# Optimization experiments

Measured on AMD Instinct MI355X. Metric: run time of the kernel, lower is better.

Reference implementation:

```python
import jax, jax.numpy as jnp
import numpy as np

N, E, C, D, A, F_, H, RNF = 20000, 200000, 14, 3, 16, 128, 128, 128
CONSTANT = 1.0
LN_EPS = 1e-5


def _pool_matrix(n_channel, dtype):
    ones = np.ones((n_channel, n_channel))
    mats = []
    for i in range(n_channel):
        ws = n_channel - i
        mats.append((np.triu(ones) - np.triu(ones, k=ws)) / ws)
    return jnp.asarray(np.stack(mats), dtype)  # [C, C, C]


def _scatter_mean(src, idx, n):
    s = jax.ops.segment_sum(src, idx, num_segments=n)
    cnt = jax.ops.segment_sum(jnp.ones((src.shape[0],), src.dtype), idx, num_segments=n)
    return s / jnp.maximum(cnt, 1.0).reshape((n,) + (1,) * (src.ndim - 1))


def setup_inputs() -> dict:
    key = jax.random.key(0)
    ks = jax.random.split(key, 24)
    h = jax.random.normal(ks[0], (N, F_), jnp.float32)
    x = jax.random.normal(ks[1], (N, C, D), jnp.float32)
    channel_attr = jax.random.normal(ks[2], (N, C, A), jnp.float32)
    cw = jax.random.uniform(ks[3], (N, C), jnp.float32)
    cw = cw * (jax.random.uniform(ks[4], (N, C)) > 0.3)  # some padded channels
    cw = cw.at[:, 0].set(jax.random.uniform(ks[5], (N,)) + 0.1)  # >=1 valid channel
    row = jax.random.randint(ks[6], (E,), 0, N, dtype=jnp.int32)
    col = jax.random.randint(ks[7], (E,), 0, N, dtype=jnp.int32)

    def lin(k, din, dout):
        return 0.02 * jax.random.normal(k, (din, dout), jnp.float32), jnp.zeros((dout,), jnp.float32)

    rad_w, rad_b = lin(ks[8], A * A, RNF)
    e_w1, e_b1 = lin(ks[9], 2 * F_ + RNF, H)
    e_w2, e_b2 = lin(ks[10], H, H)
    att_w, att_b = lin(ks[11], H, 1)
    c_w1, c_b1 = lin(ks[12], H, H)
    c_w2, c_b2 = lin(ks[13], H, C)
    n_w1, n_b1 = lin(ks[14], F_ + H, H)
    n_w2, n_b2 = lin(ks[15], H, F_)
    ln_g = jnp.ones((F_,), jnp.float32)
    ln_b = jnp.zeros((F_,), jnp.float32)
    return dict(h=h, x=x, channel_attr=channel_attr, channel_weights=cw, row=row, col=col,
                rad_w=rad_w, rad_b=rad_b, e_w1=e_w1, e_b1=e_b1, e_w2=e_w2, e_b2=e_b2,
                att_w=att_w, att_b=att_b, c_w1=c_w1, c_b1=c_b1, c_w2=c_w2, c_b2=c_b2,
                n_w1=n_w1, n_b1=n_b1, n_w2=n_w2, n_b2=n_b2, ln_g=ln_g, ln_b=ln_b)


def reference(h, x, channel_attr, channel_weights, row, col,
              rad_w, rad_b, e_w1, e_b1, e_w2, e_b2, att_w, att_b,
              c_w1, c_b1, c_w2, c_b2, n_w1, n_b1, n_w2, n_b2, ln_g, ln_b):
    silu = jax.nn.silu
    n_nodes = h.shape[0]

    # ---- coord2radial (NUM_SEG = 1) ----
    # pairwise channel distances per edge: [E, C, C]
    coord_msg = jnp.linalg.norm(x[row][:, :, None, :] - x[col][:, None, :, :], axis=-1)
    coord_msg = coord_msg * (channel_weights[row][:, :, None] * channel_weights[col][:, None, :])
    # attr^T @ msg @ attr -> [E, A, A] -> [E, A*A]
    radial = jnp.einsum('eca,ecd,edb->eab', channel_attr[row], coord_msg, channel_attr[col])
    radial = radial.reshape(radial.shape[0], -1)
    radial_norm = jnp.linalg.norm(radial, axis=-1, keepdims=True) + CONSTANT
    radial = (radial @ rad_w + rad_b) / radial_norm

    channel_mask = (channel_weights != 0).astype(x.dtype)  # [N, C]
    channel_sum = jnp.sum(channel_weights != 0, axis=-1).astype(jnp.int32)  # [N]
    pooled_col = (x[col] * channel_mask[col][:, :, None]).sum(1) / channel_sum[col].astype(x.dtype)[:, None]
    coord_diff = x[row] - pooled_col[:, None, :]  # [E, C, 3]

    # ---- edge MLP + attention gate ----
    ef = silu(jnp.concatenate([h[row], h[col], radial], axis=-1) @ e_w1 + e_b1)
    ef = silu(ef @ e_w2 + e_b2)
    ef = ef * jax.nn.sigmoid(ef @ att_w + att_b)  # att_mlp active (hidden_nf == input_nf)

    # ---- RollerPooling on coord_mlp output ----
    cm = silu(ef @ c_w1 + c_b1) @ c_w2 + c_b2  # [E, C]
    pool_mat = _pool_matrix(C, ef.dtype)[channel_sum[row] - 1]  # [E, C, C]
    pooled = jnp.einsum('eij,ej->ei', pool_mat, cm)  # [E, C]
    trans = coord_diff * pooled[:, :, None]  # [E, C, 3]

    x_new = x + _scatter_mean(trans, row, n_nodes)
    agg = _scatter_mean(ef, col, n_nodes)

    nh = silu(jnp.concatenate([h, agg], axis=-1) @ n_w1 + n_b1) @ n_w2 + n_b2
    hr = h + nh
    mu = hr.mean(-1, keepdims=True)
    var = ((hr - mu) ** 2).mean(-1, keepdims=True)
    h_new = (hr - mu) * jax.lax.rsqrt(var + LN_EPS) * ln_g + ln_b
    return h_new, x_new
```

## Files before the change

kernel.cpp:

```cpp
#include <hip/hip_runtime.h>
#include <hip/hip_bf16.h>


#define TM 64
#define TN 16
#define PAD 36

typedef __attribute__((ext_vector_type(8))) short bf16x8;
typedef __attribute__((ext_vector_type(4))) short bf16x4;
typedef __attribute__((ext_vector_type(4))) float f32x4;

__device__ __forceinline__ float siluf(float v) { return v / (1.f + __expf(-v)); }
__device__ __forceinline__ float sigmf(float v) { return 1.f / (1.f + __expf(-v)); }
__device__ __forceinline__ short f2bs(float f) {
  union { __hip_bfloat16 b; short s; } u;
  u.b = __float2bfloat16(f);
  return u.s;
}
__device__ __forceinline__ __hip_bfloat162 mk_bf162(float v0, float v1) {
  __hip_bfloat162 r;
  r.x = __float2bfloat16(v0);
  r.y = __float2bfloat16(v1);
  return r;
}

__global__ __launch_bounds__(256) void k_pack(
    const float* __restrict__ h, const float* __restrict__ x,
    const float* __restrict__ attr, const float* __restrict__ cw,
    const float* __restrict__ rad_w, const float* __restrict__ e_w1,
    const float* __restrict__ e_w2, const float* __restrict__ c_w1,
    const float* __restrict__ n_w1, const float* __restrict__ n_w2,
    const float* __restrict__ c_w2,
    __hip_bfloat16* __restrict__ wz_rad, __hip_bfloat16* __restrict__ wz_e1,
    __hip_bfloat16* __restrict__ wz_e2, __hip_bfloat16* __restrict__ wz_c1,
    __hip_bfloat16* __restrict__ wz_n1, __hip_bfloat16* __restrict__ wz_n2,
    __hip_bfloat16* __restrict__ wz_c2,
    __hip_bfloat16* __restrict__ attrS, __hip_bfloat16* __restrict__ hb,
    float* __restrict__ pooled_x, int* __restrict__ chsum, int Nn) {
  int idx = blockIdx.x * 256 + threadIdx.x;
  if (idx < 165888) {
    int i = idx;
    if (i >= 163840) {
      int base = i - 163840;
      int k = base >> 4, n = base & 15;
      wz_c2[(size_t)(k >> 5) * 512 + n * 32 + (k & 31)] =
          (n < 14) ? __float2bfloat16(c_w2[k * 14 + n]) : __float2bfloat16(0.f);
      return;
    }
    const float* W;
    __hip_bfloat16* O;
    int base;
    if (i < 32768) { W = rad_w; O = wz_rad; base = i; }
    else if (i < 81920) { W = e_w1; O = wz_e1; base = i - 32768; }
    else if (i < 98304) { W = e_w2; O = wz_e2; base = i - 81920; }
    else if (i < 114688) { W = c_w1; O = wz_c1; base = i - 98304; }
    else if (i < 147456) { W = n_w1; O = wz_n1; base = i - 114688; }
    else { W = n_w2; O = wz_n2; base = i - 147456; }
    int k = base >> 7, n = base & 127;
    int nr_ = ((n >> 5) << 5) | ((n & 1) << 4) | ((n & 31) >> 1);
    O[(size_t)((k >> 5) * 128 + nr_) * 32 + (k & 31)] = __float2bfloat16(W[base]);
    return;
  }
  idx -= 165888;
  int na = Nn * 256, nh = Nn * 128;
  if (idx < na) {
    int n = idx >> 8, r = idx & 255, i2 = r >> 4, a = r & 15;
    float v = 0.f;
    if (i2 < 14) v = attr[(size_t)n * 224 + i2 * 16 + a] * cw[(size_t)n * 14 + i2];
    attrS[(size_t)n * 256 + a * 16 + i2] = __float2bfloat16(v);
    return;
  }
  idx -= na;
  if (idx < nh) {
    hb[idx] = __float2bfloat16(h[idx]);
    return;
  }
  idx -= nh;
  if (idx >= Nn) return;
  int n = idx;
  int cnt = 0;
  float sx = 0.f, sy = 0.f, sz = 0.f;
#pragma unroll
  for (int c = 0; c < 14; c++) {
    float w = cw[n * 14 + c];
    if (w != 0.f) {
      cnt++;
      sx += x[n * 42 + c * 3 + 0];
      sy += x[n * 42 + c * 3 + 1];
      sz += x[n * 42 + c * 3 + 2];
    }
  }
  chsum[n] = cnt;
  float inv = 1.f / (float)(cnt > 0 ? cnt : 1);
  pooled_x[n * 3 + 0] = sx * inv;
  pooled_x[n * 3 + 1] = sy * inv;
  pooled_x[n * 3 + 2] = sz * inv;
}

__global__ __launch_bounds__(256, 3) void k_mega(
    const __hip_bfloat16* __restrict__ hb, const float* __restrict__ x,
    const __hip_bfloat16* __restrict__ attrS,
    const int* __restrict__ row, const int* __restrict__ col,
    const float* __restrict__ pooled_x, const int* __restrict__ chsum,
    const __hip_bfloat16* __restrict__ wz_rad, const float* __restrict__ rad_b,
    const __hip_bfloat16* __restrict__ wz_e1, const float* __restrict__ e_b1,
    const __hip_bfloat16* __restrict__ wz_e2, const float* __restrict__ e_b2,
    const float* __restrict__ att_w, const float* __restrict__ att_b,
    const __hip_bfloat16* __restrict__ wz_c1, const float* __restrict__ c_b1,
    const __hip_bfloat16* __restrict__ wz_c2, const float* __restrict__ c_b2,
    unsigned* __restrict__ cnt_row, unsigned* __restrict__ cnt_col,
    __hip_bfloat162* __restrict__ x_acc, __hip_bfloat162* __restrict__ agg,
    int Ee) {
  __shared__ __hip_bfloat16 S[12][TM][32];
  __shared__ float s_att[TM];
  __shared__ float s_red[4][TM];
  __shared__ float s_rn[TM];
  __shared__ int s_row[TM], s_col[TM], s_cs[TM];
  float* s_cm   = (float*)&S[0][0][0];
  float* s_pool = (float*)&S[1][0][0];

  const int t = threadIdx.x;
  const int e0 = blockIdx.x * TM;
  const int ne = min(TM, Ee - e0);
  const int lane = t & 63, wave = t >> 6, quad = lane >> 4, mr = lane & 15;
  const int n0 = wave * 32;
  const f32x4 zacc = {0.f, 0.f, 0.f, 0.f};
  const bf16x4 zero4 = {0, 0, 0, 0};

  if (t < TM) {
    int ge = e0 + min(t, ne - 1);
    int r = row[ge], c = col[ge];
    s_row[t] = r;
    s_col[t] = c;
    s_cs[t] = chsum[r];
    if (t < ne) {
      atomicAdd(&cnt_row[r], 1u);
      atomicAdd(&cnt_col[c], 1u);
    }
  }

#pragma unroll 1
  for (int b = 0; b < 4; b++) {
    float xr0v[4], xr1v[4], xr2v[4], xc0v[4], xc1v[4], xc2v[4];
    bf16x4 bCv[4], aRv[4];
#pragma unroll
    for (int p = 0; p < 4; p++) {
      const int e = wave * 16 + b * 4 + p;
      const int ge = e0 + min(e, ne - 1);
      const int re = row[ge], ce = col[ge];
      const int mrc = min(mr, 13);
      const float* xp = x + (size_t)re * 42 + mrc * 3;
      xr0v[p] = xp[0]; xr1v[p] = xp[1]; xr2v[p] = xp[2];
      const float* xq = x + (size_t)ce * 42 + mrc * 3;
      xc0v[p] = xq[0]; xc1v[p] = xq[1]; xc2v[p] = xq[2];
      bCv[p] = *(const bf16x4*)&attrS[(size_t)ce * 256 + mr * 16 + quad * 4];
      aRv[p] = *(const bf16x4*)&attrS[(size_t)re * 256 + mr * 16 + quad * 4];
    }
#pragma unroll
    for (int p = 0; p < 4; p++) {
      const int e = wave * 16 + b * 4 + p;
      const float xr0 = xr0v[p], xr1 = xr1v[p], xr2 = xr2v[p];
      const float xc0 = xc0v[p], xc1 = xc1v[p], xc2 = xc2v[p];
      const float nr = xr0 * xr0 + xr1 * xr1 + xr2 * xr2;
      const float nc = xc0 * xc0 + xc1 * xc1 + xc2 * xc2;
      bf16x4 aX = zero4, bX = zero4;
      if (quad == 0) {
        aX[0] = f2bs(xc0); aX[1] = f2bs(xc1); aX[2] = f2bs(xc2);
        bX[0] = f2bs(xr0); bX[1] = f2bs(xr1); bX[2] = f2bs(xr2);
      }
      f32x4 G = __builtin_amdgcn_mfma_f32_16x16x16bf16_1k(aX, bX, zacc, 0, 0, 0);
      bf16x4 aM;
#pragma unroll
      for (int r = 0; r < 4; r++) {
        float ncj = __shfl(nc, quad * 4 + r);
        aM[r] = f2bs(sqrtf(fmaxf(ncj + nr - 2.f * G[r], 0.f)));
      }
      f32x4 m1 = __builtin_amdgcn_mfma_f32_16x16x16bf16_1k(aM, bCv[p], zacc, 0, 0, 0);
      bf16x4 bM;
#pragma unroll
      for (int r = 0; r < 4; r++) bM[r] = f2bs(m1[r]);
      f32x4 rd = __builtin_amdgcn_mfma_f32_16x16x16bf16_1k(aRv[p], bM, zacc, 0, 0, 0);
      float ss = rd[0] * rd[0] + rd[1] * rd[1] + rd[2] * rd[2] + rd[3] * rd[3];
      ss += __shfl_xor(ss, 32); ss += __shfl_xor(ss, 16); ss += __shfl_xor(ss, 8);
      ss += __shfl_xor(ss, 4);  ss += __shfl_xor(ss, 2);  ss += __shfl_xor(ss, 1);
      if (lane == 0) s_rn[e] = sqrtf(ss) + 1.0f;
#pragma unroll
      for (int r = 0; r < 4; r++) {
        const int aa = quad * 4 + r;
        const int c = ((aa & 1) << 4) | mr;
        const int pcol = (((c >> 3) ^ ((e >> 1) & 3)) << 3) | (c & 7);
        S[aa >> 1][e][pcol] = __float2bfloat16(rd[r]);
      }
    }
  }
  __syncthreads();

  const int acol = ((quad ^ ((mr >> 1) & 3)) << 3);
  const int m2 = 2 * mr;

  {
    f32x4 a0[4], a1[4];
#pragma unroll
    for (int mf = 0; mf < 4; mf++) { a0[mf] = zacc; a1[mf] = zacc; }
#pragma unroll
    for (int kb = 0; kb < 8; kb++) {
      const __hip_bfloat16* wp = wz_rad + ((size_t)(kb * 128 + n0 + mr) * 32 + quad * 8);
      bf16x8 b0 = *(const bf16x8*)wp;
      bf16x8 b1 = *(const bf16x8*)(wp + 16 * 32);
#pragma unroll
      for (int mf = 0; mf < 4; mf++) {
        bf16x8 a = *(const bf16x8*)&S[kb][mf * 16 + mr][acol];
        a0[mf] = __builtin_amdgcn_mfma_f32_16x16x32_bf16(a, b0, a0[mf], 0, 0, 0);
        a1[mf] = __builtin_amdgcn_mfma_f32_16x16x32_bf16(a, b1, a1[mf], 0, 0, 0);
      }
    }
    const float2 rbp = *(const float2*)&rad_b[n0 + m2];
#pragma unroll
    for (int mf = 0; mf < 4; mf++)
#pragma unroll
      for (int r = 0; r < 4; r++) {
        int e = mf * 16 + quad * 4 + r;
        int pc2 = ((((m2) >> 3) ^ ((e >> 1) & 3)) << 3) | (m2 & 7);
        float inv = 1.f / s_rn[e];
        *(__hip_bfloat162*)&S[8 + wave][e][pc2] =
            mk_bf162((a0[mf][r] + rbp.x) * inv, (a1[mf][r] + rbp.y) * inv);
      }
  }
  __syncthreads();

  {
    const int m = t >> 2, part = t & 3;
    const int pc = ((part ^ ((m >> 1) & 3)) << 3);
    const __hip_bfloat16* hr = hb + (size_t)s_row[m] * 128 + part * 8;
    const __hip_bfloat16* hc = hb + (size_t)s_col[m] * 128 + part * 8;
#pragma unroll
    for (int kb = 0; kb < 4; kb++) {
      *(int4*)&S[kb][m][pc]     = *(const int4*)&hr[kb * 32];
      *(int4*)&S[4 + kb][m][pc] = *(const int4*)&hc[kb * 32];
    }
  }
  __syncthreads();

  f32x4 s1a0[4], s1a1[4];
#pragma unroll
  for (int mf = 0; mf < 4; mf++) { s1a0[mf] = zacc; s1a1[mf] = zacc; }
#pragma unroll
  for (int kb = 0; kb < 12; kb++) {
    const __hip_bfloat16* wp = wz_e1 + ((size_t)(kb * 128 + n0 + mr) * 32 + quad * 8);
    bf16x8 b0 = *(const bf16x8*)wp;
    bf16x8 b1 = *(const bf16x8*)(wp + 16 * 32);
#pragma unroll
    for (int mf = 0; mf < 4; mf++) {
      bf16x8 a = *(const bf16x8*)&S[kb][mf * 16 + mr][acol];
      s1a0[mf] = __builtin_amdgcn_mfma_f32_16x16x32_bf16(a, b0, s1a0[mf], 0, 0, 0);
      s1a1[mf] = __builtin_amdgcn_mfma_f32_16x16x32_bf16(a, b1, s1a1[mf], 0, 0, 0);
    }
  }
  __syncthreads();
  {
    const float2 b1p = *(const float2*)&e_b1[n0 + m2];
#pragma unroll
    for (int mf = 0; mf < 4; mf++)
#pragma unroll
      for (int r = 0; r < 4; r++) {
        int e = mf * 16 + quad * 4 + r;
        int pc2 = (((m2 >> 3) ^ ((e >> 1) & 3)) << 3) | (m2 & 7);
        *(__hip_bfloat162*)&S[wave][e][pc2] =
            mk_bf162(siluf(s1a0[mf][r] + b1p.x), siluf(s1a1[mf][r] + b1p.y));
      }
  }
  __syncthreads();

  const float2 awp = *(const float2*)&att_w[n0 + m2];
  {
    f32x4 a0[4], a1[4];
#pragma unroll
    for (int mf = 0; mf < 4; mf++) { a0[mf] = zacc; a1[mf] = zacc; }
#pragma unroll
    for (int kb = 0; kb < 4; kb++) {
      const __hip_bfloat16* wp = wz_e2 + ((size_t)(kb * 128 + n0 + mr) * 32 + quad * 8);
      bf16x8 b0 = *(const bf16x8*)wp;
      bf16x8 b1 = *(const bf16x8*)(wp + 16 * 32);
#pragma unroll
      for (int mf = 0; mf < 4; mf++) {
        bf16x8 a = *(const bf16x8*)&S[kb][mf * 16 + mr][acol];
        a0[mf] = __builtin_amdgcn_mfma_f32_16x16x32_bf16(a, b0, a0[mf], 0, 0, 0);
        a1[mf] = __builtin_amdgcn_mfma_f32_16x16x32_bf16(a, b1, a1[mf], 0, 0, 0);
      }
    }
    const float2 b2p = *(const float2*)&e_b2[n0 + m2];
    float part[4][4];
#pragma unroll
    for (int mf = 0; mf < 4; mf++)
#pragma unroll
      for (int r = 0; r < 4; r++) {
        int e = mf * 16 + quad * 4 + r;
        int pc2 = (((m2 >> 3) ^ ((e >> 1) & 3)) << 3) | (m2 & 7);
        float v0 = siluf(a0[mf][r] + b2p.x);
        float v1 = siluf(a1[mf][r] + b2p.y);
        *(__hip_bfloat162*)&S[4 + wave][e][pc2] = mk_bf162(v0, v1);
        part[mf][r] = v0 * awp.x + v1 * awp.y;
      }
#pragma unroll
    for (int msk = 1; msk < 16; msk <<= 1)
#pragma unroll
      for (int mf = 0; mf < 4; mf++)
#pragma unroll
        for (int r = 0; r < 4; r++) part[mf][r] += __shfl_xor(part[mf][r], msk);
    if (mr == 0) {
#pragma unroll
      for (int mf = 0; mf < 4; mf++)
#pragma unroll
        for (int r = 0; r < 4; r++)
          s_red[wave][mf * 16 + quad * 4 + r] = part[mf][r];
    }
  }
  __syncthreads();
  if (t < TM) {
    float s = s_red[0][t] + s_red[1][t] + s_red[2][t] + s_red[3][t];
    s_att[t] = sigmf(s + att_b[0]);
  }
  __syncthreads();

  {
    f32x4 a0[4], a1[4];
#pragma unroll
    for (int mf = 0; mf < 4; mf++) { a0[mf] = zacc; a1[mf] = zacc; }
#pragma unroll
    for (int kb = 0; kb < 4; kb++) {
      const __hip_bfloat16* wp = wz_c1 + ((size_t)(kb * 128 + n0 + mr) * 32 + quad * 8);
      bf16x8 b0 = *(const bf16x8*)wp;
      bf16x8 b1 = *(const bf16x8*)(wp + 16 * 32);
#pragma unroll
      for (int mf = 0; mf < 4; mf++) {
        bf16x8 a = *(const bf16x8*)&S[4 + kb][mf * 16 + mr][acol];
        a0[mf] = __builtin_amdgcn_mfma_f32_16x16x32_bf16(a, b0, a0[mf], 0, 0, 0);
        a1[mf] = __builtin_amdgcn_mfma_f32_16x16x32_bf16(a, b1, a1[mf], 0, 0, 0);
      }
    }
    const float2 cbp = *(const float2*)&c_b1[n0 + m2];
#pragma unroll
    for (int mf = 0; mf < 4; mf++)
#pragma unroll
      for (int r = 0; r < 4; r++) {
        int e = mf * 16 + quad * 4 + r;
        int pc2 = (((m2 >> 3) ^ ((e >> 1) & 3)) << 3) | (m2 & 7);
        float av = s_att[e];
        *(__hip_bfloat162*)&S[8 + wave][e][pc2] =
            mk_bf162(siluf(av * a0[mf][r] + cbp.x), siluf(av * a1[mf][r] + cbp.y));
      }
  }
  __syncthreads();

  {
    f32x4 acc = zacc;
#pragma unroll
    for (int kb = 0; kb < 4; kb++) {
      bf16x8 a = *(const bf16x8*)&S[8 + kb][wave * 16 + mr][acol];
      bf16x8 b = *(const bf16x8*)(wz_c2 + ((size_t)(kb * 16 + mr) * 32 + quad * 8));
      acc = __builtin_amdgcn_mfma_f32_16x16x32_bf16(a, b, acc, 0, 0, 0);
    }
    if (mr < 14) {
      float bias = c_b2[mr];
#pragma unroll
      for (int r = 0; r < 4; r++)
        s_cm[(wave * 16 + quad * 4 + r) * 14 + mr] = acc[r] + bias;
    }
  }
  __syncthreads();

  for (int i = t; i < TM * 14; i += 256) {
    int e = i / 14, c = i % 14;
    int wsz = 15 - s_cs[e];
    int hi = min(c + wsz, 14);
    float s = 0.f;
    for (int j = c; j < hi; j++) s += s_cm[e * 14 + j];
    s_pool[e * 14 + c] = s / (float)wsz;
  }
  __syncthreads();

  for (int i = t; i < TM * 21; i += 256) {
    int e = i / 21, pr = i % 21;
    if (e < ne) {
      int r0 = pr * 2, r1 = r0 + 1;
      const float* xp = x + (size_t)s_row[e] * 42;
      const float* pc = pooled_x + (size_t)s_col[e] * 3;
      float v0 = (xp[r0] - pc[r0 % 3]) * s_pool[e * 14 + r0 / 3];
      float v1 = (xp[r1] - pc[r1 % 3]) * s_pool[e * 14 + r1 / 3];
      unsafeAtomicAdd(&x_acc[(size_t)s_row[e] * 21 + pr], mk_bf162(v0, v1));
    }
  }
  for (int i = t; i < TM * 64; i += 256) {
    int e = i >> 6, o2 = i & 63;
    if (e < ne) {
      float av = s_att[e];
      int c = (o2 & 15) * 2;
      int pc = (((c >> 3) ^ ((e >> 1) & 3)) << 3) | (c & 7);
      const __hip_bfloat16* wp2 = &S[4 + (o2 >> 4)][e][pc];
      float v0 = __bfloat162float(wp2[0]) * av;
      float v1 = __bfloat162float(wp2[1]) * av;
      unsafeAtomicAdd(&agg[(size_t)s_col[e] * 64 + o2], mk_bf162(v0, v1));
    }
  }
}

__global__ __launch_bounds__(256) void k_node(
    const float* __restrict__ h, const __hip_bfloat162* __restrict__ agg,
    const unsigned* __restrict__ cnt_col,
    const __hip_bfloat16* __restrict__ wz_n1, const float* __restrict__ n_b1,
    const __hip_bfloat16* __restrict__ wz_n2, const float* __restrict__ n_b2,
    const float* __restrict__ ln_g, const float* __restrict__ ln_b,
    const float* __restrict__ x, const __hip_bfloat162* __restrict__ x_acc,
    const unsigned* __restrict__ cnt_row,
    float* __restrict__ out_h, float* __restrict__ out_x, int Nn) {
  __shared__ __hip_bfloat16 sA[8][16][PAD];
  __shared__ __hip_bfloat16 sT[4][16][PAD];
  __shared__ float s_h[TN][128];
  __shared__ float s_o[TN][132];
  const int t = threadIdx.x;
  const int nb0 = blockIdx.x * TN;
  const int nn = min(TN, Nn - nb0);

  for (int i = t; i < TN * 21; i += 256) {
    int n = i / 21, pr = i % 21;
    if (n < nn) {
      int gn = nb0 + n;
      unsigned c = cnt_row[gn];
      float inv = 1.f / (float)(c > 0 ? c : 1);
      float2 xa = __bfloat1622float2(x_acc[(size_t)gn * 21 + pr]);
      size_t gi = (size_t)gn * 42 + pr * 2;
      out_x[gi]     = x[gi] + xa.x * inv;
      out_x[gi + 1] = x[gi + 1] + xa.y * inv;
    }
  }

  for (int i = t; i < TN * 64; i += 256) {
    int m = i >> 6, kp = (i & 63) << 1;
    int kb = kp >> 5, kk = kp & 31;
    int gn = nb0 + min(m, nn - 1);
    const float2 hv = *(const float2*)&h[(size_t)gn * 128 + kp];
    sA[kb][m][kk]     = __float2bfloat16(hv.x);
    sA[kb][m][kk + 1] = __float2bfloat16(hv.y);
    s_h[m][kp]     = hv.x;
    s_h[m][kp + 1] = hv.y;
    unsigned c = cnt_col[gn];
    float inv = 1.f / (float)(c > 0 ? c : 1);
    float2 gv = __bfloat1622float2(agg[(size_t)gn * 64 + (kp >> 1)]);
    sA[4 + kb][m][kk]     = __float2bfloat16(gv.x * inv);
    sA[4 + kb][m][kk + 1] = __float2bfloat16(gv.y * inv);
  }
  __syncthreads();
  const int lane = t & 63, wave = t >> 6, quad = lane >> 4, mr = lane & 15;
  const int n0 = wave * 32;
  const int m2 = 2 * mr;
  f32x4 zacc = {0.f, 0.f, 0.f, 0.f};
  {
    f32x4 acc0 = zacc, acc1 = zacc;
#pragma unroll
    for (int kb = 0; kb < 8; kb++) {
      bf16x8 a = *(const bf16x8*)&sA[kb][mr][quad * 8];
      const __hip_bfloat16* wp = wz_n1 + ((size_t)(kb * 128 + n0 + mr) * 32 + quad * 8);
      bf16x8 b0 = *(const bf16x8*)wp;
      bf16x8 b1 = *(const bf16x8*)(wp + 16 * 32);
      acc0 = __builtin_amdgcn_mfma_f32_16x16x32_bf16(a, b0, acc0, 0, 0, 0);
      acc1 = __builtin_amdgcn_mfma_f32_16x16x32_bf16(a, b1, acc1, 0, 0, 0);
    }
    const float2 b1p = *(const float2*)&n_b1[n0 + m2];
#pragma unroll
    for (int r = 0; r < 4; r++) {
      int m = quad * 4 + r;
      *(__hip_bfloat162*)&sT[wave][m][m2] =
          mk_bf162(siluf(acc0[r] + b1p.x), siluf(acc1[r] + b1p.y));
    }
  }
  __syncthreads();
  {
    f32x4 acc0 = zacc, acc1 = zacc;
#pragma unroll
    for (int kb = 0; kb < 4; kb++) {
      bf16x8 a = *(const bf16x8*)&sT[kb][mr][quad * 8];
      const __hip_bfloat16* wp = wz_n2 + ((size_t)(kb * 128 + n0 + mr) * 32 + quad * 8);
      bf16x8 b0 = *(const bf16x8*)wp;
      bf16x8 b1 = *(const bf16x8*)(wp + 16 * 32);
      acc0 = __builtin_amdgcn_mfma_f32_16x16x32_bf16(a, b0, acc0, 0, 0, 0);
      acc1 = __builtin_amdgcn_mfma_f32_16x16x32_bf16(a, b1, acc1, 0, 0, 0);
    }
    const float2 b2p = *(const float2*)&n_b2[n0 + m2];
#pragma unroll
    for (int r = 0; r < 4; r++) {
      int m = quad * 4 + r;
      s_o[m][n0 + m2]     = s_h[m][n0 + m2] + acc0[r] + b2p.x;
      s_o[m][n0 + m2 + 1] = s_h[m][n0 + m2 + 1] + acc1[r] + b2p.y;
    }
  }
  __syncthreads();
  {
    int n = t >> 4, p = t & 15;
    float v[8];
    float s = 0.f;
#pragma unroll
    for (int j = 0; j < 8; j++) {
      v[j] = s_o[n][p * 8 + j];
      s += v[j];
    }
    s += __shfl_xor(s, 1); s += __shfl_xor(s, 2);
    s += __shfl_xor(s, 4); s += __shfl_xor(s, 8);
    float mu = s * (1.f / 128.f);
    float var = 0.f;
#pragma unroll
    for (int j = 0; j < 8; j++) {
      float d = v[j] - mu;
      var += d * d;
    }
    var += __shfl_xor(var, 1); var += __shfl_xor(var, 2);
    var += __shfl_xor(var, 4); var += __shfl_xor(var, 8);
    float rs = rsqrtf(var * (1.f / 128.f) + 1e-5f);
    if (n < nn) {
      size_t base = (size_t)(nb0 + n) * 128 + p * 8;
#pragma unroll
      for (int j = 0; j < 8; j++)
        out_h[base + j] = (v[j] - mu) * rs * ln_g[p * 8 + j] + ln_b[p * 8 + j];
    }
  }
}

extern "C" void kernel_launch(void* const* d_in, const int* in_sizes, int n_in,
                              void* d_out, int out_size, void* d_ws, size_t ws_size,
                              hipStream_t stream) {
  const float* h     = (const float*)d_in[0];
  const float* x     = (const float*)d_in[1];
  const float* attr  = (const float*)d_in[2];
  const float* cw    = (const float*)d_in[3];
  const int*   row   = (const int*)d_in[4];
  const int*   col   = (const int*)d_in[5];
  const float* rad_w = (const float*)d_in[6];
  const float* rad_b = (const float*)d_in[7];
  const float* e_w1  = (const float*)d_in[8];
  const float* e_b1  = (const float*)d_in[9];
  const float* e_w2  = (const float*)d_in[10];
  const float* e_b2  = (const float*)d_in[11];
  const float* att_w = (const float*)d_in[12];
  const float* att_b = (const float*)d_in[13];
  const float* c_w1  = (const float*)d_in[14];
  const float* c_b1  = (const float*)d_in[15];
  const float* c_w2  = (const float*)d_in[16];
  const float* c_b2  = (const float*)d_in[17];
  const float* n_w1  = (const float*)d_in[18];
  const float* n_b1  = (const float*)d_in[19];
  const float* n_w2  = (const float*)d_in[20];
  const float* n_b2  = (const float*)d_in[21];
  const float* ln_g  = (const float*)d_in[22];
  const float* ln_b  = (const float*)d_in[23];

  const int N = in_sizes[0] / 128;
  const int E = in_sizes[4];

  char* ws = (char*)d_ws;
  size_t off = 0;
  auto alloc = [&](size_t bytes) {
    size_t o = off;
    off += (bytes + 255) & ~(size_t)255;
    return o;
  };
  size_t off_wzr  = alloc(32768 * sizeof(__hip_bfloat16));
  size_t off_wz1  = alloc(49152 * sizeof(__hip_bfloat16));
  size_t off_wz2  = alloc(16384 * sizeof(__hip_bfloat16));
  size_t off_wzc  = alloc(16384 * sizeof(__hip_bfloat16));
  size_t off_wzn1 = alloc(32768 * sizeof(__hip_bfloat16));
  size_t off_wzn2 = alloc(16384 * sizeof(__hip_bfloat16));
  size_t off_wzc2 = alloc(2048 * sizeof(__hip_bfloat16));
  size_t off_atS  = alloc((size_t)N * 256 * sizeof(__hip_bfloat16));
  size_t off_hb   = alloc((size_t)N * 128 * sizeof(__hip_bfloat16));
  size_t off_px   = alloc((size_t)N * 3 * sizeof(float));
  size_t off_cs   = alloc((size_t)N * sizeof(int));
  size_t off_cntr = alloc((size_t)N * sizeof(unsigned));
  size_t off_cntc = alloc((size_t)N * sizeof(unsigned));
  size_t off_xacc = alloc((size_t)N * 21 * sizeof(__hip_bfloat162));
  size_t off_agg  = alloc((size_t)N * 64 * sizeof(__hip_bfloat162));

  __hip_bfloat16* wz_rad = (__hip_bfloat16*)(ws + off_wzr);
  __hip_bfloat16* wz_e1  = (__hip_bfloat16*)(ws + off_wz1);
  __hip_bfloat16* wz_e2  = (__hip_bfloat16*)(ws + off_wz2);
  __hip_bfloat16* wz_c1  = (__hip_bfloat16*)(ws + off_wzc);
  __hip_bfloat16* wz_n1  = (__hip_bfloat16*)(ws + off_wzn1);
  __hip_bfloat16* wz_n2  = (__hip_bfloat16*)(ws + off_wzn2);
  __hip_bfloat16* wz_c2  = (__hip_bfloat16*)(ws + off_wzc2);
  __hip_bfloat16* attrS  = (__hip_bfloat16*)(ws + off_atS);
  __hip_bfloat16* hb     = (__hip_bfloat16*)(ws + off_hb);
  float* pooled_x   = (float*)(ws + off_px);
  int* chsum        = (int*)(ws + off_cs);
  unsigned* cnt_row = (unsigned*)(ws + off_cntr);
  unsigned* cnt_col = (unsigned*)(ws + off_cntc);
  __hip_bfloat162* x_acc = (__hip_bfloat162*)(ws + off_xacc);
  __hip_bfloat162* agg   = (__hip_bfloat162*)(ws + off_agg);

  (void)hipMemsetAsync(ws + off_cntr, 0, off - off_cntr, stream);

  const int pack_items = 165888 + N * 256 + N * 128 + N;
  k_pack<<<dim3((pack_items + 255) / 256), dim3(256), 0, stream>>>(
      h, x, attr, cw, rad_w, e_w1, e_w2, c_w1, n_w1, n_w2, c_w2,
      wz_rad, wz_e1, wz_e2, wz_c1, wz_n1, wz_n2, wz_c2,
      attrS, hb, pooled_x, chsum, N);
  k_mega<<<dim3((E + TM - 1) / TM), dim3(256), 0, stream>>>(
      hb, x, attrS, row, col, pooled_x, chsum,
      wz_rad, rad_b, wz_e1, e_b1, wz_e2, e_b2, att_w, att_b,
      wz_c1, c_b1, wz_c2, c_b2, cnt_row, cnt_col, x_acc, agg, E);
  k_node<<<dim3((N + TN - 1) / TN), dim3(256), 0, stream>>>(
      h, agg, cnt_col, wz_n1, n_b1, wz_n2, n_b2, ln_g, ln_b,
      x, x_acc, cnt_row, (float*)d_out, (float*)d_out + (size_t)N * 128, N);
}
```

Baseline: 349.9 us.

## Enlarge node-kernel tile to 64 rows with swizzled LDS and vectorize pack

The node kernel now processes 64 nodes per block instead of 16, so each loaded weight fragment feeds four MFMA row tiles. It reads prepacked bf16 h from the workspace, uses one XOR-swizzled shared buffer that is reused for the fp32 output, and re-reads h from global memory for the residual add. The pack kernel's attribute and h conversions now write 8 bf16 per thread with 128-bit stores. This aims to cut weight traffic, LDS footprint and thread count in the small kernels, at the cost of more registers per thread and fewer node blocks.

```diff
diff --git a/kernel.cpp b/kernel.cpp
--- a/kernel.cpp
+++ b/kernel.cpp
@@ -3,8 +3,7 @@
 
 
 #define TM 64
-#define TN 16
-#define PAD 36
+#define TN 64
 
 typedef __attribute__((ext_vector_type(8))) short bf16x8;
 typedef __attribute__((ext_vector_type(4))) short bf16x4;
@@ -62,17 +61,31 @@
     return;
   }
   idx -= 165888;
-  int na = Nn * 256, nh = Nn * 128;
+  int na = Nn * 32, nh = Nn * 16;
   if (idx < na) {
-    int n = idx >> 8, r = idx & 255, i2 = r >> 4, a = r & 15;
-    float v = 0.f;
-    if (i2 < 14) v = attr[(size_t)n * 224 + i2 * 16 + a] * cw[(size_t)n * 14 + i2];
-    attrS[(size_t)n * 256 + a * 16 + i2] = __float2bfloat16(v);
+    int n = idx >> 5, r = idx & 31, a = r >> 1, h8 = r & 1;
+    __hip_bfloat16 outv[8];
+#pragma unroll
+    for (int j = 0; j < 8; j++) {
+      int i2 = h8 * 8 + j;
+      float v = 0.f;
+      if (i2 < 14) v = attr[(size_t)n * 224 + i2 * 16 + a] * cw[(size_t)n * 14 + i2];
+      outv[j] = __float2bfloat16(v);
+    }
+    *(int4*)&attrS[(size_t)n * 256 + a * 16 + h8 * 8] = *(int4*)outv;
     return;
   }
   idx -= na;
   if (idx < nh) {
-    hb[idx] = __float2bfloat16(h[idx]);
+    int n = idx >> 4, q = idx & 15;
+    const float4 f0 = *(const float4*)&h[(size_t)n * 128 + q * 8];
+    const float4 f1 = *(const float4*)&h[(size_t)n * 128 + q * 8 + 4];
+    __hip_bfloat16 outv[8];
+    outv[0] = __float2bfloat16(f0.x); outv[1] = __float2bfloat16(f0.y);
+    outv[2] = __float2bfloat16(f0.z); outv[3] = __float2bfloat16(f0.w);
+    outv[4] = __float2bfloat16(f1.x); outv[5] = __float2bfloat16(f1.y);
+    outv[6] = __float2bfloat16(f1.z); outv[7] = __float2bfloat16(f1.w);
+    *(int4*)&hb[(size_t)n * 128 + q * 8] = *(int4*)outv;
     return;
   }
   idx -= nh;
@@ -404,8 +417,9 @@
   }
 }
 
-__global__ __launch_bounds__(256) void k_node(
-    const float* __restrict__ h, const __hip_bfloat162* __restrict__ agg,
+__global__ __launch_bounds__(256, 3) void k_node(
+    const float* __restrict__ h, const __hip_bfloat16* __restrict__ hb,
+    const __hip_bfloat162* __restrict__ agg,
     const unsigned* __restrict__ cnt_col,
     const __hip_bfloat16* __restrict__ wz_n1, const float* __restrict__ n_b1,
     const __hip_bfloat16* __restrict__ wz_n2, const float* __restrict__ n_b2,
@@ -413,13 +427,16 @@
     const float* __restrict__ x, const __hip_bfloat162* __restrict__ x_acc,
     const unsigned* __restrict__ cnt_row,
     float* __restrict__ out_h, float* __restrict__ out_x, int Nn) {
-  __shared__ __hip_bfloat16 sA[8][16][PAD];
-  __shared__ __hip_bfloat16 sT[4][16][PAD];
-  __shared__ float s_h[TN][128];
-  __shared__ float s_o[TN][132];
+  __shared__ __hip_bfloat16 S[12][TN][32];
+  float* s_o = (float*)&S[0][0][0];
+
   const int t = threadIdx.x;
   const int nb0 = blockIdx.x * TN;
   const int nn = min(TN, Nn - nb0);
+  const int lane = t & 63, wave = t >> 6, quad = lane >> 4, mr = lane & 15;
+  const int n0 = wave * 32;
+  const int m2 = 2 * mr;
+  const f32x4 zacc = {0.f, 0.f, 0.f, 0.f};
 
   for (int i = t; i < TN * 21; i += 256) {
     int n = i / 21, pr = i % 21;
@@ -434,73 +451,104 @@
     }
   }
 
-  for (int i = t; i < TN * 64; i += 256) {
-    int m = i >> 6, kp = (i & 63) << 1;
-    int kb = kp >> 5, kk = kp & 31;
-    int gn = nb0 + min(m, nn - 1);
-    const float2 hv = *(const float2*)&h[(size_t)gn * 128 + kp];
-    sA[kb][m][kk]     = __float2bfloat16(hv.x);
-    sA[kb][m][kk + 1] = __float2bfloat16(hv.y);
-    s_h[m][kp]     = hv.x;
-    s_h[m][kp + 1] = hv.y;
+  {
+    const int m = t >> 2, part = t & 3;
+    const int gn = nb0 + min(m, nn - 1);
+    const int pc = ((part ^ ((m >> 1) & 3)) << 3);
+    const __hip_bfloat16* hr = hb + (size_t)gn * 128 + part * 8;
     unsigned c = cnt_col[gn];
     float inv = 1.f / (float)(c > 0 ? c : 1);
-    float2 gv = __bfloat1622float2(agg[(size_t)gn * 64 + (kp >> 1)]);
-    sA[4 + kb][m][kk]     = __float2bfloat16(gv.x * inv);
-    sA[4 + kb][m][kk + 1] = __float2bfloat16(gv.y * inv);
-  }
-  __syncthreads();
-  const int lane = t & 63, wave = t >> 6, quad = lane >> 4, mr = lane & 15;
-  const int n0 = wave * 32;
-  const int m2 = 2 * mr;
-  f32x4 zacc = {0.f, 0.f, 0.f, 0.f};
-  {
-    f32x4 acc0 = zacc, acc1 = zacc;
+    const __hip_bfloat162* ag = agg + (size_t)gn * 64 + part * 4;
+#pragma unroll
+    for (int kb = 0; kb < 4; kb++) {
+      *(int4*)&S[kb][m][pc] = *(const int4*)&hr[kb * 32];
+      float2 f0 = __bfloat1622float2(ag[kb * 16 + 0]);
+      float2 f1 = __bfloat1622float2(ag[kb * 16 + 1]);
+      float2 f2 = __bfloat1622float2(ag[kb * 16 + 2]);
+      float2 f3 = __bfloat1622float2(ag[kb * 16 + 3]);
+      __hip_bfloat162 pk[4];
+      pk[0] = mk_bf162(f0.x * inv, f0.y * inv);
+      pk[1] = mk_bf162(f1.x * inv, f1.y * inv);
+      pk[2] = mk_bf162(f2.x * inv, f2.y * inv);
+      pk[3] = mk_bf162(f3.x * inv, f3.y * inv);
+      *(int4*)&S[4 + kb][m][pc] = *(int4*)pk;
+    }
+  }
+  __syncthreads();
+
+  const int acol = ((quad ^ ((mr >> 1) & 3)) << 3);
+
+  {
+    f32x4 a0[4], a1[4];
+#pragma unroll
+    for (int mf = 0; mf < 4; mf++) { a0[mf] = zacc; a1[mf] = zacc; }
 #pragma unroll
     for (int kb = 0; kb < 8; kb++) {
-      bf16x8 a = *(const bf16x8*)&sA[kb][mr][quad * 8];
       const __hip_bfloat16* wp = wz_n1 + ((size_t)(kb * 128 + n0 + mr) * 32 + quad * 8);
       bf16x8 b0 = *(const bf16x8*)wp;
       bf16x8 b1 = *(const bf16x8*)(wp + 16 * 32);
-      acc0 = __builtin_amdgcn_mfma_f32_16x16x32_bf16(a, b0, acc0, 0, 0, 0);
-      acc1 = __builtin_amdgcn_mfma_f32_16x16x32_bf16(a, b1, acc1, 0, 0, 0);
+#pragma unroll
+      for (int mf = 0; mf < 4; mf++) {
+        bf16x8 a = *(const bf16x8*)&S[kb][mf * 16 + mr][acol];
+        a0[mf] = __builtin_amdgcn_mfma_f32_16x16x32_bf16(a, b0, a0[mf], 0, 0, 0);
+        a1[mf] = __builtin_amdgcn_mfma_f32_16x16x32_bf16(a, b1, a1[mf], 0, 0, 0);
+      }
     }
     const float2 b1p = *(const float2*)&n_b1[n0 + m2];
 #pragma unroll
-    for (int r = 0; r < 4; r++) {
-      int m = quad * 4 + r;
-      *(__hip_bfloat162*)&sT[wave][m][m2] =
-          mk_bf162(siluf(acc0[r] + b1p.x), siluf(acc1[r] + b1p.y));
-    }
-  }
-  __syncthreads();
-  {
-    f32x4 acc0 = zacc, acc1 = zacc;
+    for (int mf = 0; mf < 4; mf++)
+#pragma unroll
+      for (int r = 0; r < 4; r++) {
+        int e = mf * 16 + quad * 4 + r;
+        int pc2 = (((m2 >> 3) ^ ((e >> 1) & 3)) << 3) | (m2 & 7);
+        *(__hip_bfloat162*)&S[8 + wave][e][pc2] =
+            mk_bf162(siluf(a0[mf][r] + b1p.x), siluf(a1[mf][r] + b1p.y));
+      }
+  }
+  __syncthreads();
+
+  {
+    f32x4 a0[4], a1[4];
+#pragma unroll
+    for (int mf = 0; mf < 4; mf++) { a0[mf] = zacc; a1[mf] = zacc; }
 #pragma unroll
     for (int kb = 0; kb < 4; kb++) {
-      bf16x8 a = *(const bf16x8*)&sT[kb][mr][quad * 8];
       const __hip_bfloat16* wp = wz_n2 + ((size_t)(kb * 128 + n0 + mr) * 32 + quad * 8);
       bf16x8 b0 = *(const bf16x8*)wp;
       bf16x8 b1 = *(const bf16x8*)(wp + 16 * 32);
-      acc0 = __builtin_amdgcn_mfma_f32_16x16x32_bf16(a, b0, acc0, 0, 0, 0);
-      acc1 = __builtin_amdgcn_mfma_f32_16x16x32_bf16(a, b1, acc1, 0, 0, 0);
+#pragma unroll
+      for (int mf = 0; mf < 4; mf++) {
+        bf16x8 a = *(const bf16x8*)&S[8 + kb][mf * 16 + mr][acol];
+        a0[mf] = __builtin_amdgcn_mfma_f32_16x16x32_bf16(a, b0, a0[mf], 0, 0, 0);
+        a1[mf] = __builtin_amdgcn_mfma_f32_16x16x32_bf16(a, b1, a1[mf], 0, 0, 0);
+      }
     }
     const float2 b2p = *(const float2*)&n_b2[n0 + m2];
 #pragma unroll
-    for (int r = 0; r < 4; r++) {
-      int m = quad * 4 + r;
-      s_o[m][n0 + m2]     = s_h[m][n0 + m2] + acc0[r] + b2p.x;
-      s_o[m][n0 + m2 + 1] = s_h[m][n0 + m2 + 1] + acc1[r] + b2p.y;
-    }
-  }
-  __syncthreads();
-  {
-    int n = t >> 4, p = t & 15;
+    for (int mf = 0; mf < 4; mf++)
+#pragma unroll
+      for (int r = 0; r < 4; r++) {
+        int e = mf * 16 + quad * 4 + r;
+        int s = (e & 3) ^ ((e >> 2) & 3);
+        int colp = (n0 + m2) ^ (s << 3);
+        *(float2*)&s_o[e * 128 + colp] =
+            make_float2(a0[mf][r] + b2p.x, a1[mf][r] + b2p.y);
+      }
+  }
+  __syncthreads();
+
+#pragma unroll 1
+  for (int g = 0; g < 4; g++) {
+    int n = g * 16 + (t >> 4), p = t & 15;
+    int gn = nb0 + min(n, nn - 1);
+    int sw = (n & 3) ^ ((n >> 2) & 3);
+    const float* op = s_o + n * 128 + ((p ^ sw) << 3);
+    const float* hp = h + (size_t)gn * 128 + p * 8;
     float v[8];
     float s = 0.f;
 #pragma unroll
     for (int j = 0; j < 8; j++) {
-      v[j] = s_o[n][p * 8 + j];
+      v[j] = op[j] + hp[j];
       s += v[j];
     }
     s += __shfl_xor(s, 1); s += __shfl_xor(s, 2);
@@ -516,7 +564,7 @@
     var += __shfl_xor(var, 4); var += __shfl_xor(var, 8);
     float rs = rsqrtf(var * (1.f / 128.f) + 1e-5f);
     if (n < nn) {
-      size_t base = (size_t)(nb0 + n) * 128 + p * 8;
+      size_t base = (size_t)gn * 128 + p * 8;
 #pragma unroll
       for (int j = 0; j < 8; j++)
         out_h[base + j] = (v[j] - mu) * rs * ln_g[p * 8 + j] + ln_b[p * 8 + j];
@@ -596,7 +644,7 @@
 
   (void)hipMemsetAsync(ws + off_cntr, 0, off - off_cntr, stream);
 
-  const int pack_items = 165888 + N * 256 + N * 128 + N;
+  const int pack_items = 165888 + N * 32 + N * 16 + N;
   k_pack<<<dim3((pack_items + 255) / 256), dim3(256), 0, stream>>>(
       h, x, attr, cw, rad_w, e_w1, e_w2, c_w1, n_w1, n_w2, c_w2,
       wz_rad, wz_e1, wz_e2, wz_c1, wz_n1, wz_n2, wz_c2,
@@ -606,6 +654,6 @@
       wz_rad, rad_b, wz_e1, e_b1, wz_e2, e_b2, att_w, att_b,
       wz_c1, c_b1, wz_c2, c_b2, cnt_row, cnt_col, x_acc, agg, E);
   k_node<<<dim3((N + TN - 1) / TN), dim3(256), 0, stream>>>(
-      h, agg, cnt_col, wz_n1, n_b1, wz_n2, n_b2, ln_g, ln_b,
+      h, hb, agg, cnt_col, wz_n1, n_b1, wz_n2, n_b2, ln_g, ln_b,
       x, x_acc, cnt_row, (float*)d_out, (float*)d_out + (size_t)N * 128, N);
 }
```

Result: no change. 349.4 us (-0.1%).
